# Performance work log

Hardware: AMD Instinct MI355X
Metric: run time of the kernel (lower is better)

The kernel has to match this reference:

```python
import jax, jax.numpy as jnp
import numpy as np

N_NODES = 50000
N_EDGES = 300000
D_IN = 256
D_HID = 256


def setup_inputs() -> dict:
    key = jax.random.key(0)
    ks = jax.random.split(key, 9)
    x = jax.random.normal(ks[0], (N_NODES, D_IN), dtype=jnp.float32)
    src = jax.random.randint(ks[1], (N_EDGES,), 0, N_NODES, dtype=jnp.int64)
    dst = jax.random.randint(ks[2], (N_EDGES,), 0, N_NODES, dtype=jnp.int64)
    # Kaiming-uniform-ish init like nn.Linear defaults
    def lin(k, fan_in, fan_out):
        bound = 1.0 / np.sqrt(fan_in)
        kw, kb = jax.random.split(k)
        W = jax.random.uniform(kw, (fan_out, fan_in), minval=-bound, maxval=bound, dtype=jnp.float32)
        b = jax.random.uniform(kb, (fan_out,), minval=-bound, maxval=bound, dtype=jnp.float32)
        return W, b
    W1, b1 = lin(ks[3], 2 * D_IN, D_HID)
    W2, b2 = lin(ks[4], D_HID, D_HID)
    W3, b3 = lin(ks[5], D_HID, 1)
    return {"x": x, "src": src, "dst": dst,
            "W1": W1, "b1": b1, "W2": W2, "b2": b2, "W3": W3, "b3": b3}


def reference(x, src, dst, W1, b1, W2, b2, W3, b3):
    # gather src/dst node features per edge and concat -> [E, 2*D_IN]
    h = jnp.concatenate([x[src], x[dst]], axis=1)
    h = jax.nn.relu(h @ W1.T + b1)          # [E, D_HID]
    h = jax.nn.relu(h @ W2.T + b2)          # dropout is identity in eval mode
    score = h @ W3.T + b3                   # [E, 1]
    return score
```

## Files before the change

### kernel.cpp

```cpp
#include <hip/hip_runtime.h>

typedef short bfx8 __attribute__((ext_vector_type(8)));
typedef float fx4 __attribute__((ext_vector_type(4)));

#define E_TILE 64

__device__ __forceinline__ float b2f(short s) {
  union { unsigned u; float f; } v; v.u = ((unsigned)(unsigned short)s) << 16; return v.f;
}
__device__ __forceinline__ short f2b(float f) {
  union { float f; unsigned u; } v; v.f = f;
  unsigned u = v.u;
  u += 0x7fffu + ((u >> 16) & 1u);
  return (short)(u >> 16);
}
__device__ __forceinline__ float relu(float f) { return f > 0.f ? f : 0.f; }

__global__ void k_prep(const float* __restrict__ W1, const float* __restrict__ W2,
                       unsigned short* __restrict__ B1, unsigned short* __restrict__ W2b) {
  int t = blockIdx.x * 256 + threadIdx.x;
  if (t < 512 * 256) {
    int n = t >> 8, k = t & 255;
    float v = (n < 256) ? W1[n * 512 + k] : W1[(n - 256) * 512 + 256 + k];
    B1[t] = (unsigned short)f2b(v);
  } else if (t < 512 * 256 + 256 * 256) {
    int i = t - 512 * 256;
    W2b[i] = (unsigned short)f2b(W2[i]);
  }
}

__launch_bounds__(256, 2)
__global__ void k_node(const float* __restrict__ x, const unsigned short* __restrict__ B1,
                       const float* __restrict__ b1,
                       unsigned short* __restrict__ PQ, int n_nodes) {
  __shared__ __align__(16) short smA[64 * 264];
  __shared__ __align__(16) short smT[32 * 264];
  const int tid = threadIdx.x;
  const int wave = tid >> 6, lane = tid & 63;
  const int lr = lane & 15, lg = lane >> 4;
  const int m0 = blockIdx.x * 64;

  {
    int r = tid >> 2;
    int m = m0 + r;
    bool ok = m < n_nodes;
#pragma unroll
    for (int j = 0; j < 8; ++j) {
      int c = (tid & 3) * 8 + j * 32;
      bfx8 o;
      if (ok) {
        const float* p = x + (size_t)m * 256 + c;
        float4 v0 = *(const float4*)(p);
        float4 v1 = *(const float4*)(p + 4);
        o[0] = f2b(v0.x); o[1] = f2b(v0.y); o[2] = f2b(v0.z); o[3] = f2b(v0.w);
        o[4] = f2b(v1.x); o[5] = f2b(v1.y); o[6] = f2b(v1.z); o[7] = f2b(v1.w);
      } else {
        o = (bfx8){0, 0, 0, 0, 0, 0, 0, 0};
      }
      *(bfx8*)&smA[r * 264 + c] = o;
    }
  }
  __syncthreads();

#pragma unroll
  for (int half = 0; half < 2; ++half) {
    const int n0 = half * 256 + wave * 64;

    fx4 acc[4][4] = {};
#pragma unroll
    for (int ks = 0; ks < 8; ++ks) {
      bfx8 af[4];
#pragma unroll
      for (int mt = 0; mt < 4; ++mt)
        af[mt] = *(const bfx8*)&smA[(mt * 16 + lr) * 264 + ks * 32 + lg * 8];
#pragma unroll
      for (int nt = 0; nt < 4; ++nt) {
        bfx8 bf = *(const bfx8*)(B1 + (size_t)(n0 + nt * 16 + lr) * 256 + ks * 32 + lg * 8);
#pragma unroll
        for (int mt = 0; mt < 4; ++mt)
          acc[mt][nt] = __builtin_amdgcn_mfma_f32_16x16x32_bf16(af[mt], bf, acc[mt][nt], 0, 0, 0);
      }
    }

    float bias[4];
#pragma unroll
    for (int nt = 0; nt < 4; ++nt) {
      int n = n0 + nt * 16 + lr;
      bias[nt] = half ? b1[n - 256] : 0.f;
    }

#pragma unroll
    for (int h = 0; h < 2; ++h) {
      __syncthreads();
#pragma unroll
      for (int mt2 = 0; mt2 < 2; ++mt2) {
        const int mt = 2 * h + mt2;
#pragma unroll
        for (int nt = 0; nt < 4; ++nt)
#pragma unroll
          for (int i = 0; i < 4; ++i) {
            int mr = mt2 * 16 + lg * 4 + i;
            int nc = wave * 64 + nt * 16 + lr;
            smT[mr * 264 + nc] = f2b(acc[mt][nt][i] + bias[nt]);
          }
      }
      __syncthreads();
      int r = tid >> 3, cbase = (tid & 7) * 8;
      int m = m0 + h * 32 + r;
      if (m < n_nodes) {
#pragma unroll
        for (int j = 0; j < 4; ++j) {
          int c = cbase + j * 64;
          *(bfx8*)(PQ + (size_t)m * 512 + half * 256 + c) = *(const bfx8*)&smT[r * 264 + c];
        }
      }
    }
  }
}

__launch_bounds__(256, 2)
__global__ void k_edge(const unsigned short* __restrict__ PQ,
                       const int* __restrict__ src, const int* __restrict__ dst,
                       const unsigned short* __restrict__ W2b,
                       const float* __restrict__ b2, const float* __restrict__ W3,
                       const float* __restrict__ b3, float* __restrict__ out,
                       int E, int ntiles) {
  __shared__ __align__(16) short smH[64 * 264];
  __shared__ float smS[4][64];
  const int tid = threadIdx.x;
  const int wave = tid >> 6, lane = tid & 63;
  const int lr = lane & 15, lg = lane >> 4;

  bfx8 bw[4][8];
  float b2v[4], w3v[4];
#pragma unroll
  for (int nt = 0; nt < 4; ++nt) {
    int n = wave * 64 + nt * 16 + lr;
    b2v[nt] = b2[n];
    w3v[nt] = W3[n];
#pragma unroll
    for (int ks = 0; ks < 8; ++ks)
      bw[nt][ks] = *(const bfx8*)(W2b + n * 256 + ks * 32 + lg * 8);
  }
  const float b3v = b3[0];

  for (int tile = blockIdx.x; tile < ntiles; tile += gridDim.x) {
    const int base = tile * E_TILE;
    {
      int r = tid >> 2;
      int e = base + r;
      if (e < E) {
        int s = src[e], d = dst[e];
        const unsigned short* ps = PQ + (size_t)s * 512;
        const unsigned short* pd = PQ + (size_t)d * 512 + 256;
#pragma unroll
        for (int it = 0; it < 8; ++it) {
          int c = (tid & 3) * 8 + it * 32;
          bfx8 pv = *(const bfx8*)(ps + c);
          bfx8 qv = *(const bfx8*)(pd + c);
          bfx8 o;
#pragma unroll
          for (int j = 0; j < 8; ++j)
            o[j] = f2b(relu(b2f(pv[j]) + b2f(qv[j])));
          *(bfx8*)&smH[r * 264 + c] = o;
        }
      } else {
        bfx8 z = (bfx8){0, 0, 0, 0, 0, 0, 0, 0};
#pragma unroll
        for (int it = 0; it < 8; ++it) {
          int c = (tid & 3) * 8 + it * 32;
          *(bfx8*)&smH[r * 264 + c] = z;
        }
      }
    }
    __syncthreads();

    fx4 acc[4][4] = {};
#pragma unroll
    for (int ks = 0; ks < 8; ++ks) {
      bfx8 af[4];
#pragma unroll
      for (int mt = 0; mt < 4; ++mt)
        af[mt] = *(const bfx8*)&smH[(mt * 16 + lr) * 264 + ks * 32 + lg * 8];
#pragma unroll
      for (int nt = 0; nt < 4; ++nt)
#pragma unroll
        for (int mt = 0; mt < 4; ++mt)
          acc[mt][nt] = __builtin_amdgcn_mfma_f32_16x16x32_bf16(af[mt], bw[nt][ks], acc[mt][nt], 0, 0, 0);
    }

#pragma unroll
    for (int mt = 0; mt < 4; ++mt)
#pragma unroll
      for (int i = 0; i < 4; ++i) {
        float p = 0.f;
#pragma unroll
        for (int nt = 0; nt < 4; ++nt)
          p += relu(acc[mt][nt][i] + b2v[nt]) * w3v[nt];
        p += __shfl_xor(p, 1);
        p += __shfl_xor(p, 2);
        p += __shfl_xor(p, 4);
        p += __shfl_xor(p, 8);
        if (lr == 0) smS[wave][mt * 16 + lg * 4 + i] = p;
      }
    __syncthreads();
    if (tid < 64) {
      int e = base + tid;
      if (e < E) out[e] = smS[0][tid] + smS[1][tid] + smS[2][tid] + smS[3][tid] + b3v;
    }
    __syncthreads();
  }
}

__global__ void k_fallback(const float* __restrict__ x, const int* __restrict__ src,
                           const int* __restrict__ dst, const float* __restrict__ W1,
                           const float* __restrict__ b1, const float* __restrict__ W2,
                           const float* __restrict__ b2, const float* __restrict__ W3,
                           const float* __restrict__ b3, float* __restrict__ out, int E) {
  __shared__ float smF[4][512];
  __shared__ float smG[4][256];
  int wave = threadIdx.x >> 6, lane = threadIdx.x & 63;
  int e = blockIdx.x * 4 + wave;
  bool valid = e < E;
  int ec = valid ? e : 0;
  int s = src[ec], d = dst[ec];
  for (int j = 0; j < 8; ++j) {
    int k = lane * 8 + j;
    smF[wave][k] = (k < 256) ? x[(size_t)s * 256 + k] : x[(size_t)d * 256 + k - 256];
  }
  __syncthreads();
  for (int t = 0; t < 4; ++t) {
    int n = lane + t * 64;
    float a = b1[n];
    for (int k = 0; k < 512; ++k) a += smF[wave][k] * W1[n * 512 + k];
    smG[wave][n] = relu(a);
  }
  __syncthreads();
  float p = 0.f;
  for (int t = 0; t < 4; ++t) {
    int n = lane + t * 64;
    float a = b2[n];
    for (int k = 0; k < 256; ++k) a += smG[wave][k] * W2[n * 256 + k];
    p += relu(a) * W3[n];
  }
  for (int m = 1; m < 64; m <<= 1) p += __shfl_xor(p, m);
  if (lane == 0 && valid) out[e] = p + b3[0];
}

extern "C" void kernel_launch(void* const* d_in, const int* in_sizes, int n_in,
                              void* d_out, int out_size, void* d_ws, size_t ws_size,
                              hipStream_t stream) {
  const float* x  = (const float*)d_in[0];
  const int*   src = (const int*)d_in[1];
  const int*   dst = (const int*)d_in[2];
  const float* W1 = (const float*)d_in[3];
  const float* b1 = (const float*)d_in[4];
  const float* W2 = (const float*)d_in[5];
  const float* b2 = (const float*)d_in[6];
  const float* W3 = (const float*)d_in[7];
  const float* b3 = (const float*)d_in[8];
  float* out = (float*)d_out;

  const int E = in_sizes[1];
  const int n_nodes = in_sizes[0] / 256;

  const size_t offB1 = 0;
  const size_t offW2 = (size_t)512 * 256 * 2;
  const size_t offPQ = offW2 + (size_t)256 * 256 * 2;
  const size_t need = offPQ + (size_t)n_nodes * 512 * 2;

  if (ws_size >= need) {
    unsigned short* B1  = (unsigned short*)((char*)d_ws + offB1);
    unsigned short* W2b = (unsigned short*)((char*)d_ws + offW2);
    unsigned short* PQ  = (unsigned short*)((char*)d_ws + offPQ);
    k_prep<<<768, 256, 0, stream>>>(W1, W2, B1, W2b);
    k_node<<<(n_nodes + 63) / 64, 256, 0, stream>>>(x, B1, b1, PQ, n_nodes);
    const int ntiles = (E + E_TILE - 1) / E_TILE;
    k_edge<<<512, 256, 0, stream>>>(PQ, src, dst, W2b, b2, W3, b3, out, E, ntiles);
  } else {
    k_fallback<<<(E + 3) / 4, 256, 0, stream>>>(x, src, dst, W1, b1, W2, b2, W3, b3, out, E);
  }
}
```

Measured before the change: 219.7 us.

## Persist node GEMM with register-resident W1, prefetch edge indices, cheaper bf16 add

The node kernel becomes a persistent 512-thread kernel. Each of its 8 waves keeps its slice of the concatenated W1 weights in registers across tiles and computes all 512 output columns in one pass, instead of reloading B1 from global memory per k-step for each of two halves. The transpose buffer is aliased onto the input shared buffer to save LDS, at the cost of extra barriers. The edge kernel prefetches the next tile's src/dst indices and replaces the per-element bf16 decode/encode with bit masks and a perm-based pack that rounds half-up instead of to nearest-even.

```diff
diff --git a/kernel.cpp b/kernel.cpp
--- a/kernel.cpp
+++ b/kernel.cpp
@@ -5,9 +5,6 @@
 
 #define E_TILE 64
 
-__device__ __forceinline__ float b2f(short s) {
-  union { unsigned u; float f; } v; v.u = ((unsigned)(unsigned short)s) << 16; return v.f;
-}
 __device__ __forceinline__ short f2b(float f) {
   union { float f; unsigned u; } v; v.f = f;
   unsigned u = v.u;
@@ -15,6 +12,8 @@
   return (short)(u >> 16);
 }
 __device__ __forceinline__ float relu(float f) { return f > 0.f ? f : 0.f; }
+__device__ __forceinline__ float asf(unsigned u) { union { unsigned u; float f; } v; v.u = u; return v.f; }
+__device__ __forceinline__ unsigned asu(float f) { union { float f; unsigned u; } v; v.f = f; return v.u; }
 
 __global__ void k_prep(const float* __restrict__ W1, const float* __restrict__ W2,
                        unsigned short* __restrict__ B1, unsigned short* __restrict__ W2b) {
@@ -29,42 +28,53 @@
   }
 }
 
-__launch_bounds__(256, 2)
+__launch_bounds__(512, 2)
 __global__ void k_node(const float* __restrict__ x, const unsigned short* __restrict__ B1,
                        const float* __restrict__ b1,
-                       unsigned short* __restrict__ PQ, int n_nodes) {
+                       unsigned short* __restrict__ PQ, int n_nodes, int ntiles) {
   __shared__ __align__(16) short smA[64 * 264];
-  __shared__ __align__(16) short smT[32 * 264];
+  short* smT = smA;
   const int tid = threadIdx.x;
   const int wave = tid >> 6, lane = tid & 63;
   const int lr = lane & 15, lg = lane >> 4;
-  const int m0 = blockIdx.x * 64;
-
-  {
-    int r = tid >> 2;
-    int m = m0 + r;
-    bool ok = m < n_nodes;
-#pragma unroll
-    for (int j = 0; j < 8; ++j) {
-      int c = (tid & 3) * 8 + j * 32;
-      bfx8 o;
-      if (ok) {
-        const float* p = x + (size_t)m * 256 + c;
-        float4 v0 = *(const float4*)(p);
-        float4 v1 = *(const float4*)(p + 4);
-        o[0] = f2b(v0.x); o[1] = f2b(v0.y); o[2] = f2b(v0.z); o[3] = f2b(v0.w);
-        o[4] = f2b(v1.x); o[5] = f2b(v1.y); o[6] = f2b(v1.z); o[7] = f2b(v1.w);
-      } else {
-        o = (bfx8){0, 0, 0, 0, 0, 0, 0, 0};
-      }
-      *(bfx8*)&smA[r * 264 + c] = o;
-    }
-  }
-  __syncthreads();
-
-#pragma unroll
-  for (int half = 0; half < 2; ++half) {
-    const int n0 = half * 256 + wave * 64;
+  const int n0 = wave * 64;
+
+  bfx8 bw[4][8];
+  float bias[4];
+#pragma unroll
+  for (int nt = 0; nt < 4; ++nt) {
+    int n = n0 + nt * 16 + lr;
+    bias[nt] = (n >= 256) ? b1[n - 256] : 0.f;
+#pragma unroll
+    for (int ks = 0; ks < 8; ++ks)
+      bw[nt][ks] = *(const bfx8*)(B1 + (size_t)n * 256 + ks * 32 + lg * 8);
+  }
+
+  for (int tile = blockIdx.x; tile < ntiles; tile += gridDim.x) {
+    const int m0 = tile * 64;
+    __syncthreads();
+
+    {
+      int r = tid >> 3, sub = tid & 7;
+      int m = m0 + r;
+      bool ok = m < n_nodes;
+#pragma unroll
+      for (int j = 0; j < 4; ++j) {
+        int c = sub * 8 + j * 64;
+        bfx8 o;
+        if (ok) {
+          const float* p = x + (size_t)m * 256 + c;
+          float4 v0 = *(const float4*)(p);
+          float4 v1 = *(const float4*)(p + 4);
+          o[0] = f2b(v0.x); o[1] = f2b(v0.y); o[2] = f2b(v0.z); o[3] = f2b(v0.w);
+          o[4] = f2b(v1.x); o[5] = f2b(v1.y); o[6] = f2b(v1.z); o[7] = f2b(v1.w);
+        } else {
+          o = (bfx8){0, 0, 0, 0, 0, 0, 0, 0};
+        }
+        *(bfx8*)&smA[r * 264 + c] = o;
+      }
+    }
+    __syncthreads();
 
     fx4 acc[4][4] = {};
 #pragma unroll
@@ -74,24 +84,15 @@
       for (int mt = 0; mt < 4; ++mt)
         af[mt] = *(const bfx8*)&smA[(mt * 16 + lr) * 264 + ks * 32 + lg * 8];
 #pragma unroll
-      for (int nt = 0; nt < 4; ++nt) {
-        bfx8 bf = *(const bfx8*)(B1 + (size_t)(n0 + nt * 16 + lr) * 256 + ks * 32 + lg * 8);
+      for (int nt = 0; nt < 4; ++nt)
 #pragma unroll
         for (int mt = 0; mt < 4; ++mt)
-          acc[mt][nt] = __builtin_amdgcn_mfma_f32_16x16x32_bf16(af[mt], bf, acc[mt][nt], 0, 0, 0);
-      }
-    }
-
-    float bias[4];
-#pragma unroll
-    for (int nt = 0; nt < 4; ++nt) {
-      int n = n0 + nt * 16 + lr;
-      bias[nt] = half ? b1[n - 256] : 0.f;
-    }
+          acc[mt][nt] = __builtin_amdgcn_mfma_f32_16x16x32_bf16(af[mt], bw[nt][ks], acc[mt][nt], 0, 0, 0);
+    }
+    __syncthreads();
 
 #pragma unroll
     for (int h = 0; h < 2; ++h) {
-      __syncthreads();
 #pragma unroll
       for (int mt2 = 0; mt2 < 2; ++mt2) {
         const int mt = 2 * h + mt2;
@@ -100,20 +101,21 @@
 #pragma unroll
           for (int i = 0; i < 4; ++i) {
             int mr = mt2 * 16 + lg * 4 + i;
-            int nc = wave * 64 + nt * 16 + lr;
-            smT[mr * 264 + nc] = f2b(acc[mt][nt][i] + bias[nt]);
+            int nc = n0 + nt * 16 + lr;
+            smT[mr * 520 + nc] = f2b(acc[mt][nt][i] + bias[nt]);
           }
       }
       __syncthreads();
-      int r = tid >> 3, cbase = (tid & 7) * 8;
+      int r = tid >> 4, cbase = (tid & 15) * 8;
       int m = m0 + h * 32 + r;
       if (m < n_nodes) {
 #pragma unroll
         for (int j = 0; j < 4; ++j) {
-          int c = cbase + j * 64;
-          *(bfx8*)(PQ + (size_t)m * 512 + half * 256 + c) = *(const bfx8*)&smT[r * 264 + c];
+          int c = cbase + j * 128;
+          *(bfx8*)(PQ + (size_t)m * 512 + c) = *(const bfx8*)&smT[r * 520 + c];
         }
       }
+      __syncthreads();
     }
   }
 }
@@ -144,35 +146,47 @@
   }
   const float b3v = b3[0];
 
+  const int r = tid >> 2;
+  const int sub = tid & 3;
+  const int stride = gridDim.x * E_TILE;
+
+  int e0 = blockIdx.x * E_TILE + r;
+  int s_cur = 0, d_cur = 0;
+  if (e0 < E) { s_cur = src[e0]; d_cur = dst[e0]; }
+
   for (int tile = blockIdx.x; tile < ntiles; tile += gridDim.x) {
     const int base = tile * E_TILE;
-    {
-      int r = tid >> 2;
-      int e = base + r;
-      if (e < E) {
-        int s = src[e], d = dst[e];
-        const unsigned short* ps = PQ + (size_t)s * 512;
-        const unsigned short* pd = PQ + (size_t)d * 512 + 256;
-#pragma unroll
-        for (int it = 0; it < 8; ++it) {
-          int c = (tid & 3) * 8 + it * 32;
-          bfx8 pv = *(const bfx8*)(ps + c);
-          bfx8 qv = *(const bfx8*)(pd + c);
-          bfx8 o;
-#pragma unroll
-          for (int j = 0; j < 8; ++j)
-            o[j] = f2b(relu(b2f(pv[j]) + b2f(qv[j])));
-          *(bfx8*)&smH[r * 264 + c] = o;
+    const int e = base + r;
+    if (e < E) {
+      const unsigned* ps = (const unsigned*)(PQ + (size_t)s_cur * 512);
+      const unsigned* pd = (const unsigned*)(PQ + (size_t)d_cur * 512 + 256);
+#pragma unroll
+      for (int it = 0; it < 8; ++it) {
+        int c = sub * 8 + it * 32;
+        uint4 pv = *(const uint4*)(ps + (c >> 1));
+        uint4 qv = *(const uint4*)(pd + (c >> 1));
+        unsigned o[4];
+        const unsigned* pw = (const unsigned*)&pv;
+        const unsigned* qw = (const unsigned*)&qv;
+#pragma unroll
+        for (int w = 0; w < 4; ++w) {
+          unsigned up = pw[w], uq = qw[w];
+          float slo = relu(asf(up << 16) + asf(uq << 16));
+          float shi = relu(asf(up & 0xffff0000u) + asf(uq & 0xffff0000u));
+          o[w] = __builtin_amdgcn_perm(asu(shi) + 0x8000u, asu(slo) + 0x8000u,
+                                       0x07060302u);
         }
-      } else {
-        bfx8 z = (bfx8){0, 0, 0, 0, 0, 0, 0, 0};
-#pragma unroll
-        for (int it = 0; it < 8; ++it) {
-          int c = (tid & 3) * 8 + it * 32;
-          *(bfx8*)&smH[r * 264 + c] = z;
-        }
-      }
-    }
+        *(uint4*)&smH[r * 264 + c] = make_uint4(o[0], o[1], o[2], o[3]);
+      }
+    } else {
+#pragma unroll
+      for (int it = 0; it < 8; ++it) {
+        int c = sub * 8 + it * 32;
+        *(uint4*)&smH[r * 264 + c] = make_uint4(0, 0, 0, 0);
+      }
+    }
+    int e_next = e + stride;
+    if (e_next < E) { s_cur = src[e_next]; d_cur = dst[e_next]; }
     __syncthreads();
 
     fx4 acc[4][4] = {};
@@ -205,8 +219,8 @@
       }
     __syncthreads();
     if (tid < 64) {
-      int e = base + tid;
-      if (e < E) out[e] = smS[0][tid] + smS[1][tid] + smS[2][tid] + smS[3][tid] + b3v;
+      int eo = base + tid;
+      if (eo < E) out[eo] = smS[0][tid] + smS[1][tid] + smS[2][tid] + smS[3][tid] + b3v;
     }
     __syncthreads();
   }
@@ -274,7 +288,8 @@
     unsigned short* W2b = (unsigned short*)((char*)d_ws + offW2);
     unsigned short* PQ  = (unsigned short*)((char*)d_ws + offPQ);
     k_prep<<<768, 256, 0, stream>>>(W1, W2, B1, W2b);
-    k_node<<<(n_nodes + 63) / 64, 256, 0, stream>>>(x, B1, b1, PQ, n_nodes);
+    const int ntiles_n = (n_nodes + 63) / 64;
+    k_node<<<256, 512, 0, stream>>>(x, B1, b1, PQ, n_nodes, ntiles_n);
     const int ntiles = (E + E_TILE - 1) / E_TILE;
     k_edge<<<512, 256, 0, stream>>>(PQ, src, dst, W2b, b2, W3, b3, out, E, ntiles);
   } else {
```

Result: slower. 229.8 us (+4.6%).
